# Kernel optimization log

Measured on AMD Instinct MI355X. Metric: run time of the kernel, lower is better.

## Reference

```python
import jax, jax.numpy as jnp
import numpy as np

N = 8192
E = 262144
D_IN = 256
D_OUT = 256

def setup_inputs() -> dict:
    key = jax.random.key(0)
    k1, k2, k3, k4 = jax.random.split(key, 4)
    x = jax.random.normal(k1, (N, D_IN), dtype=jnp.float32)
    edge_index = jax.random.randint(k2, (2, E), 0, N, dtype=jnp.int64)
    W = jax.random.normal(k3, (D_OUT, D_IN), dtype=jnp.float32) * (1.0 / np.sqrt(D_IN))
    b = jax.random.normal(k4, (D_OUT,), dtype=jnp.float32) * 0.01
    return {"x": x, "edge_index": edge_index, "W": W, "b": b}

def reference(x, edge_index, W, b):
    num_nodes = x.shape[0]
    # dense adjacency: adj[src, dst] = 1.0 (duplicates collapse to 1, matching torch assignment)
    adj = jnp.zeros((num_nodes, num_nodes), dtype=x.dtype)
    adj = adj.at[edge_index[0], edge_index[1]].set(1.0)
    adj = adj + jnp.eye(num_nodes, dtype=x.dtype)  # self-loops (may yield 2.0 if edge had self-loop, as in torch)
    deg = adj.sum(axis=1, keepdims=True)           # [N, 1]
    adj_norm = adj / deg                           # row-normalized
    aggregated = adj_norm @ x                      # [N, D_IN]
    return aggregated @ W.T + b                    # linear: [N, D_OUT]
```

## Files before the change

kernel.cpp:

```cpp
#include <hip/hip_runtime.h>
#include <hip/hip_fp16.h>


#define NNODES 8192
#define DFEAT  256
#define WPR    256
#define LISTCAP 256

typedef __attribute__((ext_vector_type(8))) _Float16 f16x8;
typedef __attribute__((ext_vector_type(4))) _Float16 f16x4;
typedef __attribute__((ext_vector_type(4))) float    f32x4;

__global__ __launch_bounds__(256) void gcn_gemm(
    const float* __restrict__ X, const float* __restrict__ W,
    _Float16* __restrict__ Y, uint4* __restrict__ bitmap4) {
  const int bid = blockIdx.x, tid = threadIdx.x;
  const int gtid = bid * 256 + tid;

  {
    const uint4 z = {0u, 0u, 0u, 0u};
#pragma unroll
    for (int i = 0; i < 8; ++i) bitmap4[(size_t)gtid * 8 + i] = z;
  }

  const int wave = tid >> 6, lane = tid & 63;
  const int row0 = (bid >> 1) * 64 + wave * 16;
  const int col0 = (bid & 1) * 128;
  const int lr = lane & 15;
  const int kh = (lane >> 4) * 8;

  f32x4 acc[8];
#pragma unroll
  for (int i = 0; i < 8; ++i) acc[i] = (f32x4){0.f, 0.f, 0.f, 0.f};

  const float* ap = X + (size_t)(row0 + lr) * DFEAT + kh;
  const float* wp = W + (size_t)(col0 + lr) * DFEAT + kh;

#pragma unroll
  for (int k0 = 0; k0 < DFEAT; k0 += 32) {
    float4 x0 = *(const float4*)(ap + k0);
    float4 x1 = *(const float4*)(ap + k0 + 4);
    f16x8 a = {(_Float16)x0.x, (_Float16)x0.y, (_Float16)x0.z, (_Float16)x0.w,
               (_Float16)x1.x, (_Float16)x1.y, (_Float16)x1.z, (_Float16)x1.w};
#pragma unroll
    for (int nt = 0; nt < 8; ++nt) {
      float4 w0 = *(const float4*)(wp + k0 + nt * 16 * DFEAT);
      float4 w1 = *(const float4*)(wp + k0 + nt * 16 * DFEAT + 4);
      f16x8 bh = {(_Float16)w0.x, (_Float16)w0.y, (_Float16)w0.z, (_Float16)w0.w,
                  (_Float16)w1.x, (_Float16)w1.y, (_Float16)w1.z, (_Float16)w1.w};
      f16x8 bl = {(_Float16)(w0.x - (float)bh[0]), (_Float16)(w0.y - (float)bh[1]),
                  (_Float16)(w0.z - (float)bh[2]), (_Float16)(w0.w - (float)bh[3]),
                  (_Float16)(w1.x - (float)bh[4]), (_Float16)(w1.y - (float)bh[5]),
                  (_Float16)(w1.z - (float)bh[6]), (_Float16)(w1.w - (float)bh[7])};
      acc[nt] = __builtin_amdgcn_mfma_f32_16x16x32_f16(a, bh, acc[nt], 0, 0, 0);
      acc[nt] = __builtin_amdgcn_mfma_f32_16x16x32_f16(a, bl, acc[nt], 0, 0, 0);
    }
  }

  const int crow = row0 + (lane >> 4) * 4;
  const int ccol = col0 + lr;
#pragma unroll
  for (int nt = 0; nt < 8; ++nt)
#pragma unroll
    for (int r = 0; r < 4; ++r)
      Y[(size_t)(crow + r) * DFEAT + ccol + nt * 16] = (_Float16)acc[nt][r];
}

__global__ __launch_bounds__(256) void gcn_scatter(
    const int* __restrict__ ei, int E, unsigned* __restrict__ bitmap) {
  int e = blockIdx.x * 256 + threadIdx.x;
  if (e < E) {
    int s = ei[e];
    int d = ei[E + e];
    atomicOr(&bitmap[(size_t)s * WPR + (d >> 5)], 1u << (d & 31));
  }
}

__global__ __launch_bounds__(256) void gcn_aggregate(
    const unsigned* __restrict__ bitmap, const _Float16* __restrict__ Y,
    const float* __restrict__ bias, float* __restrict__ out) {
  __shared__ unsigned short listS[4][LISTCAP];
  __shared__ int cntS[4];

  const int tid = threadIdx.x;
  const int wave = tid >> 6, lane = tid & 63;
  const int node = blockIdx.x * 4 + wave;
  unsigned short* list = listS[wave];

  if (lane == 0) cntS[wave] = 0;
  uint4 wv = *(const uint4*)(bitmap + (size_t)node * WPR + lane * 4);
  unsigned ws[4] = {wv.x, wv.y, wv.z, wv.w};
#pragma unroll
  for (int q = 0; q < 4; ++q) {
    unsigned w = ws[q];
    int base = (lane * 4 + q) * 32;
    while (w) {
      int bit = __ffs(w) - 1;
      w &= w - 1;
      int pos = atomicAdd(&cntS[wave], 1);
      if (pos < LISTCAP) list[pos] = (unsigned short)(base + bit);
    }
  }
  __syncthreads();

  const int n = min(cntS[wave], LISTCAP);
  const int ch4 = lane * 4;

  f16x4 sv = *(const f16x4*)(Y + (size_t)node * DFEAT + ch4);
  f32x4 a0 = {(float)sv[0], (float)sv[1], (float)sv[2], (float)sv[3]};
  f32x4 a1 = {0.f, 0.f, 0.f, 0.f}, a2 = a1, a3 = a1;

  int k = 0;
  for (; k + 4 <= n; k += 4) {
    int j0 = list[k], j1 = list[k + 1], j2 = list[k + 2], j3 = list[k + 3];
    f16x4 r0 = *(const f16x4*)(Y + (size_t)j0 * DFEAT + ch4);
    f16x4 r1 = *(const f16x4*)(Y + (size_t)j1 * DFEAT + ch4);
    f16x4 r2 = *(const f16x4*)(Y + (size_t)j2 * DFEAT + ch4);
    f16x4 r3 = *(const f16x4*)(Y + (size_t)j3 * DFEAT + ch4);
#pragma unroll
    for (int c = 0; c < 4; ++c) {
      a0[c] += (float)r0[c]; a1[c] += (float)r1[c];
      a2[c] += (float)r2[c]; a3[c] += (float)r3[c];
    }
  }
  for (; k < n; ++k) {
    f16x4 r0 = *(const f16x4*)(Y + (size_t)list[k] * DFEAT + ch4);
#pragma unroll
    for (int c = 0; c < 4; ++c) a0[c] += (float)r0[c];
  }

  const float inv = 1.f / (float)(n + 1);
  const float4 b4 = *(const float4*)(bias + ch4);
  float4 o;
  o.x = (a0[0] + a1[0] + a2[0] + a3[0]) * inv + b4.x;
  o.y = (a0[1] + a1[1] + a2[1] + a3[1]) * inv + b4.y;
  o.z = (a0[2] + a1[2] + a2[2] + a3[2]) * inv + b4.z;
  o.w = (a0[3] + a1[3] + a2[3] + a3[3]) * inv + b4.w;
  *(float4*)(out + (size_t)node * DFEAT + ch4) = o;
}

extern "C" void kernel_launch(void* const* d_in, const int* in_sizes, int n_in,
                              void* d_out, int out_size, void* d_ws, size_t ws_size,
                              hipStream_t stream) {
  const float* x  = (const float*)d_in[0];
  const int*   ei = (const int*)d_in[1];
  const float* W  = (const float*)d_in[2];
  const float* b  = (const float*)d_in[3];
  float* out = (float*)d_out;
  const int E = in_sizes[1] / 2;

  char* p = (char*)d_ws;
  size_t off = 0;
  auto take = [&](size_t bytes) { char* r = p + off; off = (off + bytes + 255) & ~(size_t)255; return r; };
  unsigned* bitmap = (unsigned*) take((size_t)NNODES * WPR * 4);
  _Float16* Y      = (_Float16*) take((size_t)NNODES * DFEAT * 2);

  gcn_gemm<<<256, 256, 0, stream>>>(x, W, Y, (uint4*)bitmap);
  gcn_scatter<<<(E + 255) / 256, 256, 0, stream>>>(ei, E, bitmap);
  gcn_aggregate<<<NNODES / 4, 256, 0, stream>>>(bitmap, Y, b, out);
}
```

Before: 108.6 us.

## Retile GEMM to 512 blocks, stage output via LDS, use nontemporal stores

The GEMM grid doubles to 512 blocks, each computing a 64x64 tile instead of 64x128, so more CUs have work. Output is staged through padded shared memory so Y is written as coalesced 16-byte rows. The bitmap zeroing is spread across the larger grid with coalesced strided nontemporal stores, and the final output store is also nontemporal. The aim is better store coalescing and occupancy, at the cost of each block loading W rows again and a block-level sync.

```diff
diff --git a/kernel.cpp b/kernel.cpp
--- a/kernel.cpp
+++ b/kernel.cpp
@@ -6,35 +6,36 @@
 #define DFEAT  256
 #define WPR    256
 #define LISTCAP 256
+#define LPAD   72
 
 typedef __attribute__((ext_vector_type(8))) _Float16 f16x8;
 typedef __attribute__((ext_vector_type(4))) _Float16 f16x4;
 typedef __attribute__((ext_vector_type(4))) float    f32x4;
+typedef __attribute__((ext_vector_type(4))) unsigned u32x4;
 
 __global__ __launch_bounds__(256) void gcn_gemm(
     const float* __restrict__ X, const float* __restrict__ W,
-    _Float16* __restrict__ Y, uint4* __restrict__ bitmap4) {
+    _Float16* __restrict__ Y, u32x4* __restrict__ bitmap4) {
   const int bid = blockIdx.x, tid = threadIdx.x;
-  const int gtid = bid * 256 + tid;
 
   {
-    const uint4 z = {0u, 0u, 0u, 0u};
+    const u32x4 z = {0u, 0u, 0u, 0u};
+    const int g = bid * 256 + tid;
 #pragma unroll
-    for (int i = 0; i < 8; ++i) bitmap4[(size_t)gtid * 8 + i] = z;
+    for (int i = 0; i < 4; ++i)
+      __builtin_nontemporal_store(z, &bitmap4[(size_t)g + (size_t)i * 131072]);
   }
 
   const int wave = tid >> 6, lane = tid & 63;
-  const int row0 = (bid >> 1) * 64 + wave * 16;
-  const int col0 = (bid & 1) * 128;
-  const int lr = lane & 15;
-  const int kh = (lane >> 4) * 8;
+  const int R0 = (bid >> 2) * 64, C0 = (bid & 3) * 64;
+  const int lr = lane & 15, kh = (lane >> 4) * 8;
 
-  f32x4 acc[8];
+  f32x4 acc[4];
 #pragma unroll
-  for (int i = 0; i < 8; ++i) acc[i] = (f32x4){0.f, 0.f, 0.f, 0.f};
+  for (int i = 0; i < 4; ++i) acc[i] = (f32x4){0.f, 0.f, 0.f, 0.f};
 
-  const float* ap = X + (size_t)(row0 + lr) * DFEAT + kh;
-  const float* wp = W + (size_t)(col0 + lr) * DFEAT + kh;
+  const float* ap = X + (size_t)(R0 + wave * 16 + lr) * DFEAT + kh;
+  const float* wp = W + (size_t)(C0 + lr) * DFEAT + kh;
 
 #pragma unroll
   for (int k0 = 0; k0 < DFEAT; k0 += 32) {
@@ -43,7 +44,7 @@
     f16x8 a = {(_Float16)x0.x, (_Float16)x0.y, (_Float16)x0.z, (_Float16)x0.w,
                (_Float16)x1.x, (_Float16)x1.y, (_Float16)x1.z, (_Float16)x1.w};
 #pragma unroll
-    for (int nt = 0; nt < 8; ++nt) {
+    for (int nt = 0; nt < 4; ++nt) {
       float4 w0 = *(const float4*)(wp + k0 + nt * 16 * DFEAT);
       float4 w1 = *(const float4*)(wp + k0 + nt * 16 * DFEAT + 4);
       f16x8 bh = {(_Float16)w0.x, (_Float16)w0.y, (_Float16)w0.z, (_Float16)w0.w,
@@ -57,13 +58,23 @@
     }
   }
 
-  const int crow = row0 + (lane >> 4) * 4;
-  const int ccol = col0 + lr;
+  __shared__ __align__(16) _Float16 tile[64][LPAD];
+  const int rbase = wave * 16 + (lane >> 4) * 4;
 #pragma unroll
-  for (int nt = 0; nt < 8; ++nt)
+  for (int nt = 0; nt < 4; ++nt)
 #pragma unroll
     for (int r = 0; r < 4; ++r)
-      Y[(size_t)(crow + r) * DFEAT + ccol + nt * 16] = (_Float16)acc[nt][r];
+      tile[rbase + r][nt * 16 + lr] = (_Float16)acc[nt][r];
+  __syncthreads();
+
+#pragma unroll
+  for (int it = 0; it < 2; ++it) {
+    int c = tid + it * 256;
+    int row = c >> 3, seg = c & 7;
+    u32x4 v = *(const u32x4*)&tile[row][seg * 8];
+    __builtin_nontemporal_store(
+        v, (u32x4*)(Y + (size_t)(R0 + row) * DFEAT + C0 + seg * 8));
+  }
 }
 
 __global__ __launch_bounds__(256) void gcn_scatter(
@@ -131,12 +142,12 @@
 
   const float inv = 1.f / (float)(n + 1);
   const float4 b4 = *(const float4*)(bias + ch4);
-  float4 o;
-  o.x = (a0[0] + a1[0] + a2[0] + a3[0]) * inv + b4.x;
-  o.y = (a0[1] + a1[1] + a2[1] + a3[1]) * inv + b4.y;
-  o.z = (a0[2] + a1[2] + a2[2] + a3[2]) * inv + b4.z;
-  o.w = (a0[3] + a1[3] + a2[3] + a3[3]) * inv + b4.w;
-  *(float4*)(out + (size_t)node * DFEAT + ch4) = o;
+  f32x4 o;
+  o[0] = (a0[0] + a1[0] + a2[0] + a3[0]) * inv + b4.x;
+  o[1] = (a0[1] + a1[1] + a2[1] + a3[1]) * inv + b4.y;
+  o[2] = (a0[2] + a1[2] + a2[2] + a3[2]) * inv + b4.z;
+  o[3] = (a0[3] + a1[3] + a2[3] + a3[3]) * inv + b4.w;
+  __builtin_nontemporal_store(o, (f32x4*)(out + (size_t)node * DFEAT + ch4));
 }
 
 extern "C" void kernel_launch(void* const* d_in, const int* in_sizes, int n_in,
@@ -155,7 +166,7 @@
   unsigned* bitmap = (unsigned*) take((size_t)NNODES * WPR * 4);
   _Float16* Y      = (_Float16*) take((size_t)NNODES * DFEAT * 2);
 
-  gcn_gemm<<<256, 256, 0, stream>>>(x, W, Y, (uint4*)bitmap);
+  gcn_gemm<<<512, 256, 0, stream>>>(x, W, Y, (u32x4*)bitmap);
   gcn_scatter<<<(E + 255) / 256, 256, 0, stream>>>(ei, E, bitmap);
   gcn_aggregate<<<NNODES / 4, 256, 0, stream>>>(bitmap, Y, b, out);
 }
```

New measurement: 108.7 us. No clear change (+0.1%).
